# Kernel tuning notes

Measured on AMD Instinct MI355X. Metric: run time of the kernel, lower is better.

## Reference

```python
import jax, jax.numpy as jnp
import numpy as np

B, S, D, H = 4, 2048, 1024, 16
DK = D // H


def setup_inputs() -> dict:
    key = jax.random.key(0)
    ks = jax.random.split(key, 9)
    x = jax.random.normal(ks[0], (B, S, D), dtype=jnp.float32)
    scale = 1.0 / np.sqrt(D)
    wq = jax.random.normal(ks[1], (D, D), dtype=jnp.float32) * scale
    wk = jax.random.normal(ks[2], (D, D), dtype=jnp.float32) * scale
    wv = jax.random.normal(ks[3], (D, D), dtype=jnp.float32) * scale
    wo = jax.random.normal(ks[4], (D, D), dtype=jnp.float32) * scale
    bq = jax.random.normal(ks[5], (D,), dtype=jnp.float32) * 0.01
    bk = jax.random.normal(ks[6], (D,), dtype=jnp.float32) * 0.01
    bv = jax.random.normal(ks[7], (D,), dtype=jnp.float32) * 0.01
    bo = jax.random.normal(ks[8], (D,), dtype=jnp.float32) * 0.01
    # causal mask: True where scores should be masked to -inf (j > i)
    mask = jnp.triu(jnp.ones((S, S), dtype=bool), k=1)[None, None, :, :]
    return {"x": x, "wq": wq, "bq": bq, "wk": wk, "bk": bk,
            "wv": wv, "bv": bv, "wo": wo, "bo": bo, "mask": mask}


def reference(x, wq, bq, wk, bk, wv, bv, wo, bo, mask):
    b, s, _ = x.shape
    # projections
    q = (x @ wq + bq).reshape(b, s, H, DK).transpose(0, 2, 1, 3)  # [B,H,S,DK]
    k = (x @ wk + bk).reshape(b, s, H, DK).transpose(0, 2, 1, 3)
    v = (x @ wv + bv).reshape(b, s, H, DK).transpose(0, 2, 1, 3)
    scores = jnp.einsum("bhqd,bhkd->bhqk", q, k) / np.sqrt(DK)
    scores = jnp.where(mask, -jnp.inf, scores)
    attn = jax.nn.softmax(scores, axis=-1)  # dropout p=0.0 -> identity
    out = jnp.einsum("bhqk,bhkd->bhqd", attn, v)
    out = out.transpose(0, 2, 1, 3).reshape(b, s, D)
    return out @ wo + bo
```

## Files before the change

kernel.cpp:

```cpp
#include <hip/hip_runtime.h>


typedef __attribute__((ext_vector_type(8))) short short8;
typedef __attribute__((ext_vector_type(4))) float floatx4;
typedef __attribute__((ext_vector_type(4))) unsigned short ushort4v;

#define SCLF (0.125f * 1.44269504f)

__device__ __forceinline__ unsigned short f2bf(float f) {
    unsigned int u = __float_as_uint(f);
    unsigned int r = (u + 0x7fffu + ((u >> 16) & 1u)) >> 16;
    return (unsigned short)r;
}

__device__ __forceinline__ unsigned int pk2bf(float lo, float hi) {
    return __builtin_amdgcn_perm(__float_as_uint(hi), __float_as_uint(lo), 0x07060302u);
}

__device__ __forceinline__ void gll16(const unsigned short* g, unsigned short* l) {
    __builtin_amdgcn_global_load_lds(
        (const __attribute__((address_space(1))) unsigned int*)g,
        (__attribute__((address_space(3))) unsigned int*)l, 16, 0, 0);
}

__device__ __forceinline__ void xcd_tile3(int nx, int& m0, int& n0) {
    int lid = blockIdx.y * nx + blockIdx.x;
    int grp = lid & 7;
    int inner = lid >> 3;
    int my = grp * 4 + (inner & 3);
    int mx = inner >> 2;
    m0 = my * 256;
    n0 = mx * 128;
}

__global__ void cvtx_kernel(const float* __restrict__ x, unsigned short* __restrict__ xb) {
    int i = (blockIdx.x * 256 + threadIdx.x) * 4;
    float4 v = *(const float4*)&x[i];
    ushort4v o;
    o.x = f2bf(v.x); o.y = f2bf(v.y); o.z = f2bf(v.z); o.w = f2bf(v.w);
    *(ushort4v*)&xb[i] = o;
}

__global__ void wtrans_kernel(const float* __restrict__ wq, const float* __restrict__ wk,
                              const float* __restrict__ wv, const float* __restrict__ wo,
                              unsigned short* __restrict__ wtbase) {
    __shared__ float t[32][33];
    int z = blockIdx.z;
    const float* w = (z == 0) ? wq : (z == 1) ? wk : (z == 2) ? wv : wo;
    unsigned short* wt = wtbase + ((long)z << 20);
    int kb = blockIdx.y * 32, nb = blockIdx.x * 32;
    int col = threadIdx.x & 31, rw = threadIdx.x >> 5;
#pragma unroll
    for (int i = 0; i < 4; i++) {
        int row = rw + i * 8;
        t[row][col] = w[(kb + row) * 1024 + nb + col];
    }
    __syncthreads();
#pragma unroll
    for (int i = 0; i < 4; i++) {
        int row = rw + i * 8;
        wt[(nb + row) * 1024 + kb + col] = f2bf(t[col][row]);
    }
}

#define ASZ (256 * 64)
#define BSZ (128 * 64)
#define BUFSZ (ASZ + BSZ)

__device__ __forceinline__ short8 ldsr(const unsigned short* p) { return *(const short8*)p; }

template <bool SW>
__device__ __forceinline__ void gemm_core256(const unsigned short* __restrict__ A,
                                             const unsigned short* __restrict__ Bt,
                                             unsigned short* lds,
                                             int m0, int n0, floatx4 (&acc)[8][2]) {
    const int K = 1024, NT = 16;
    int tid = threadIdx.x;
    int lane = tid & 63, wave = tid >> 6;
    int wm = wave >> 2, wn = wave & 3;
    int quad = lane >> 4, l15 = lane & 15, l7 = l15 & 7;
    int rsub = lane >> 3;
    int gl = (lane & 7) ^ rsub;

    floatx4 zero4 = {0.f, 0.f, 0.f, 0.f};
#pragma unroll
    for (int i = 0; i < 8; i++)
#pragma unroll
        for (int j = 0; j < 2; j++) acc[i][j] = zero4;

    auto stage = [&](int kt, int b) {
        const unsigned short* Ag = A + (long)m0 * K + kt * 64;
        const unsigned short* Bg = Bt + (long)n0 * K + kt * 64;
        unsigned short* as = lds + b * BUFSZ;
        unsigned short* bs = as + ASZ;
#pragma unroll
        for (int p = 0; p < 4; p++) {
            int chunk = wave * 4 + p;
            gll16(&Ag[(chunk * 8 + rsub) * K + gl * 8], &as[chunk * 512 + lane * 8]);
        }
#pragma unroll
        for (int p = 0; p < 2; p++) {
            int chunk = wave * 2 + p;
            gll16(&Bg[(chunk * 8 + rsub) * K + gl * 8], &bs[chunk * 512 + lane * 8]);
        }
    };

    stage(0, 0);
    stage(1, 1);
    stage(2, 2);
    asm volatile("s_waitcnt vmcnt(12)" ::: "memory");
    __builtin_amdgcn_s_barrier();
    asm volatile("" ::: "memory");

    int buf = 0;
    for (int kt = 0; kt < NT; kt++) {
        const unsigned short* as = lds + buf * BUFSZ;
        const unsigned short* bs = as + ASZ;
        short8 bf[2][2], af[4][2], ag[4][2];
#pragma unroll
        for (int j = 0; j < 2; j++) {
            int rb = wn * 32 + j * 16 + l15;
#pragma unroll
            for (int kk = 0; kk < 2; kk++)
                bf[j][kk] = ldsr(&bs[rb * 64 + (((kk * 4 + quad) ^ l7) * 8)]);
        }
#pragma unroll
        for (int i = 0; i < 4; i++) {
            int r = wm * 128 + i * 16 + l15;
#pragma unroll
            for (int kk = 0; kk < 2; kk++)
                af[i][kk] = ldsr(&as[r * 64 + (((kk * 4 + quad) ^ l7) * 8)]);
        }
        __builtin_amdgcn_s_setprio(1);
#pragma unroll
        for (int i = 0; i < 4; i++)
#pragma unroll
            for (int j = 0; j < 2; j++)
#pragma unroll
                for (int kk = 0; kk < 2; kk++)
                    acc[i][j] = SW
                        ? __builtin_amdgcn_mfma_f32_16x16x32_bf16(bf[j][kk], af[i][kk], acc[i][j], 0, 0, 0)
                        : __builtin_amdgcn_mfma_f32_16x16x32_bf16(af[i][kk], bf[j][kk], acc[i][j], 0, 0, 0);
        __builtin_amdgcn_s_setprio(0);
#pragma unroll
        for (int i = 0; i < 4; i++) {
            int r = wm * 128 + 64 + i * 16 + l15;
#pragma unroll
            for (int kk = 0; kk < 2; kk++)
                ag[i][kk] = ldsr(&as[r * 64 + (((kk * 4 + quad) ^ l7) * 8)]);
        }
        __builtin_amdgcn_s_setprio(1);
#pragma unroll
        for (int i = 0; i < 4; i++)
#pragma unroll
            for (int j = 0; j < 2; j++)
#pragma unroll
                for (int kk = 0; kk < 2; kk++)
                    acc[4 + i][j] = SW
                        ? __builtin_amdgcn_mfma_f32_16x16x32_bf16(bf[j][kk], ag[i][kk], acc[4 + i][j], 0, 0, 0)
                        : __builtin_amdgcn_mfma_f32_16x16x32_bf16(ag[i][kk], bf[j][kk], acc[4 + i][j], 0, 0, 0);
        __builtin_amdgcn_s_setprio(0);
        asm volatile("" ::: "memory");
        __builtin_amdgcn_s_barrier();
        asm volatile("" ::: "memory");
        if (kt + 3 < NT) {
            stage(kt + 3, buf);
            asm volatile("s_waitcnt vmcnt(12)" ::: "memory");
        } else if (kt + 3 == NT) {
            asm volatile("s_waitcnt vmcnt(6)" ::: "memory");
        } else if (kt + 2 == NT) {
            asm volatile("s_waitcnt vmcnt(0)" ::: "memory");
        }
        __builtin_amdgcn_s_barrier();
        asm volatile("" ::: "memory");
        buf = (buf == 2) ? 0 : buf + 1;
    }
}

__global__ __launch_bounds__(512, 2) void proj_kernel(
    const unsigned short* __restrict__ xb, const unsigned short* __restrict__ wt,
    const float* __restrict__ bq, const float* __restrict__ bk, const float* __restrict__ bv,
    unsigned short* __restrict__ qo, unsigned short* __restrict__ ko,
    unsigned short* __restrict__ vo) {
    extern __shared__ __align__(16) unsigned short smem[];
    int m0, n0;
    xcd_tile3(24, m0, n0);
    int tid = threadIdx.x, lane = tid & 63, wave = tid >> 6;
    int wm = wave >> 2, wn = wave & 3, quad = lane >> 4, l15 = lane & 15;
    floatx4 acc[8][2];

    if (n0 < 2048) {
        gemm_core256<true>(xb, wt, smem, m0, n0, acc);
        int which = n0 >> 10;
        const float* bias = which ? bk : bq;
        unsigned short* dst = which ? ko : qo;
        float sc = which ? 1.0f : SCLF;
#pragma unroll
        for (int mt = 0; mt < 8; mt++)
#pragma unroll
            for (int nt = 0; nt < 2; nt++) {
                int tok = m0 + wm * 128 + mt * 16 + l15;
                int b = tok >> 11, s = tok & 2047;
                int colf = (n0 + wn * 32 + nt * 16 + quad * 4) & 1023;
                float4 bb = *(const float4*)&bias[colf];
                int h = colf >> 6, dk = colf & 63;
                ushort4v o;
                o.x = f2bf((acc[mt][nt][0] + bb.x) * sc);
                o.y = f2bf((acc[mt][nt][1] + bb.y) * sc);
                o.z = f2bf((acc[mt][nt][2] + bb.z) * sc);
                o.w = f2bf((acc[mt][nt][3] + bb.w) * sc);
                *(ushort4v*)&dst[((long)((b * 16 + h) * 2048 + s)) * 64 + dk] = o;
            }
    } else {
        gemm_core256<false>(xb, wt, smem, m0, n0, acc);
#pragma unroll
        for (int mt = 0; mt < 8; mt++)
#pragma unroll
            for (int nt = 0; nt < 2; nt++) {
                int tok0 = m0 + wm * 128 + mt * 16 + quad * 4;
                int b = tok0 >> 11, s = tok0 & 2047;
                int colf = (n0 & 1023) + wn * 32 + nt * 16 + l15;
                int h = colf >> 6, dk = colf & 63;
                float bb = bv[colf];
                ushort4v o;
                o.x = f2bf(acc[mt][nt][0] + bb);
                o.y = f2bf(acc[mt][nt][1] + bb);
                o.z = f2bf(acc[mt][nt][2] + bb);
                o.w = f2bf(acc[mt][nt][3] + bb);
                *(ushort4v*)&vo[((long)((b * 16 + h) * 64 + dk)) * 2048 + s] = o;
            }
    }
}

__global__ __launch_bounds__(512, 2) void gemm_out_kernel(
    const unsigned short* __restrict__ ob, const unsigned short* __restrict__ wto,
    const float* __restrict__ bo, float* __restrict__ out) {
    extern __shared__ __align__(16) unsigned short smem[];
    int m0, n0;
    xcd_tile3(8, m0, n0);
    int tid = threadIdx.x, lane = tid & 63, wave = tid >> 6;
    int wm = wave >> 2, wn = wave & 3, quad = lane >> 4, l15 = lane & 15;
    floatx4 acc[8][2];
    gemm_core256<true>(ob, wto, smem, m0, n0, acc);

#pragma unroll
    for (int mt = 0; mt < 8; mt++)
#pragma unroll
        for (int nt = 0; nt < 2; nt++) {
            int tok = m0 + wm * 128 + mt * 16 + l15;
            int cg = n0 + wn * 32 + nt * 16 + quad * 4;
            float4 bb = *(const float4*)&bo[cg];
            float4 o;
            o.x = acc[mt][nt][0] + bb.x;
            o.y = acc[mt][nt][1] + bb.y;
            o.z = acc[mt][nt][2] + bb.z;
            o.w = acc[mt][nt][3] + bb.w;
            *(float4*)&out[(long)tok * 1024 + cg] = o;
        }
}

__device__ __forceinline__ void stage_kv(const unsigned short* __restrict__ Kg,
                                         const unsigned short* __restrict__ Vg,
                                         unsigned short* Ks, unsigned short* Vs,
                                         int lane, int wave) {
    int rsub = lane >> 3;
    int g = (lane & 7) ^ rsub;
#pragma unroll
    for (int p = 0; p < 2; p++) {
        int chunk = wave * 2 + p;
        int r = chunk * 8 + rsub;
        gll16(&Kg[r * 64 + g * 8], &Ks[chunk * 512]);
        gll16(&Vg[r * 2048 + g * 8], &Vs[chunk * 512]);
    }
}

__global__ __launch_bounds__(256, 4) void attn_kernel(
    const unsigned short* __restrict__ Q, const unsigned short* __restrict__ Kk,
    const unsigned short* __restrict__ Vt, unsigned short* __restrict__ O) {
    __shared__ __align__(16) unsigned short Ks[2][8 * 512];
    __shared__ __align__(16) unsigned short Vs[2][8 * 512];
    __shared__ __align__(16) unsigned short Ps[4 * 16 * 64];

    int bid = blockIdx.x;
    int qt = 15 - (bid >> 6);
    int bh = bid & 63;
    int q0 = qt * 128;
    long base = (long)bh * 2048 * 64;
    long vbase = (long)bh * 64 * 2048;
    int tid = threadIdx.x, lane = tid & 63, wave = tid >> 6;
    int quad = lane >> 4, l15 = lane & 15, l7 = l15 & 7;

    short8 qfA[2], qfB[2];
    int qrA = q0 + wave * 16 + l15;
    int qrB = qrA + 64;
    qfA[0] = *(const short8*)&Q[base + qrA * 64 + quad * 8];
    qfA[1] = *(const short8*)&Q[base + qrA * 64 + 32 + quad * 8];
    qfB[0] = *(const short8*)&Q[base + qrB * 64 + quad * 8];
    qfB[1] = *(const short8*)&Q[base + qrB * 64 + 32 + quad * 8];

    float lA = 0.f, lB = 0.f;
    floatx4 oA[4], oB[4];
    floatx4 zero4 = {0.f, 0.f, 0.f, 0.f};
#pragma unroll
    for (int st = 0; st < 4; st++) { oA[st] = zero4; oB[st] = zero4; }

    unsigned short* myP = &Ps[(wave * 16) * 64];
    int pw_off = l15 * 64 + (quad & 1) * 4;
    int pr0 = l15 * 64 + ((quad ^ l7) * 8);
    int pr1 = l15 * 64 + (((4 + quad) ^ l7) * 8);

    int ktmax = 2 * qt + 1;
    stage_kv(&Kk[base], &Vt[vbase], Ks[0], Vs[0], lane, wave);
    __syncthreads();

    for (int kt = 0; kt <= ktmax; kt++) {
        int cur = kt & 1;
        if (kt < ktmax)
            stage_kv(&Kk[base + (long)(kt + 1) * 64 * 64], &Vt[vbase + (kt + 1) * 64],
                     Ks[cur ^ 1], Vs[cur ^ 1], lane, wave);
        bool doA = (kt < ktmax);
        bool maskA = (kt == ktmax - 1);
        bool maskB = (kt == ktmax);

        floatx4 saA[4], saB[4];
#pragma unroll
        for (int st = 0; st < 4; st++) {
            int row = st * 16 + l15;
            short8 kf0 = ldsr(&Ks[cur][row * 64 + ((quad ^ l7) * 8)]);
            short8 kf1 = ldsr(&Ks[cur][row * 64 + (((4 + quad) ^ l7) * 8)]);
            saB[st] = __builtin_amdgcn_mfma_f32_16x16x32_bf16(kf0, qfB[0], zero4, 0, 0, 0);
            saB[st] = __builtin_amdgcn_mfma_f32_16x16x32_bf16(kf1, qfB[1], saB[st], 0, 0, 0);
            if (doA) {
                saA[st] = __builtin_amdgcn_mfma_f32_16x16x32_bf16(kf0, qfA[0], zero4, 0, 0, 0);
                saA[st] = __builtin_amdgcn_mfma_f32_16x16x32_bf16(kf1, qfA[1], saA[st], 0, 0, 0);
            }
        }

        int kg0 = kt * 64 + quad * 4;
        short8 pfB0, pfB1, pfA0, pfA1;
        {
            float p[4][4];
#pragma unroll
            for (int st = 0; st < 4; st++)
#pragma unroll
                for (int r = 0; r < 4; r++)
                    p[st][r] = __builtin_amdgcn_exp2f(saB[st][r]);
            if (maskB) {
#pragma unroll
                for (int st = 0; st < 4; st++)
#pragma unroll
                    for (int r = 0; r < 4; r++)
                        if (kg0 + st * 16 + r > qrB) p[st][r] = 0.f;
            }
            float rs = 0.f;
#pragma unroll
            for (int st = 0; st < 4; st++) {
                rs += p[st][0] + p[st][1] + p[st][2] + p[st][3];
                uint2 pw;
                pw.x = pk2bf(p[st][0], p[st][1]);
                pw.y = pk2bf(p[st][2], p[st][3]);
                *(uint2*)&myP[pw_off + (((st * 2 + (quad >> 1)) ^ l7) * 8)] = pw;
            }
            rs += __shfl_xor(rs, 16, 64);
            rs += __shfl_xor(rs, 32, 64);
            lB += rs;
            pfB0 = ldsr(&myP[pr0]);
            pfB1 = ldsr(&myP[pr1]);
        }
        if (doA) {
            float p[4][4];
#pragma unroll
            for (int st = 0; st < 4; st++)
#pragma unroll
                for (int r = 0; r < 4; r++)
                    p[st][r] = __builtin_amdgcn_exp2f(saA[st][r]);
            if (maskA) {
#pragma unroll
                for (int st = 0; st < 4; st++)
#pragma unroll
                    for (int r = 0; r < 4; r++)
                        if (kg0 + st * 16 + r > qrA) p[st][r] = 0.f;
            }
            float rs = 0.f;
#pragma unroll
            for (int st = 0; st < 4; st++) {
                rs += p[st][0] + p[st][1] + p[st][2] + p[st][3];
                uint2 pw;
                pw.x = pk2bf(p[st][0], p[st][1]);
                pw.y = pk2bf(p[st][2], p[st][3]);
                *(uint2*)&myP[pw_off + (((st * 2 + (quad >> 1)) ^ l7) * 8)] = pw;
            }
            rs += __shfl_xor(rs, 16, 64);
            rs += __shfl_xor(rs, 32, 64);
            lA += rs;
            pfA0 = ldsr(&myP[pr0]);
            pfA1 = ldsr(&myP[pr1]);
        }

#pragma unroll
        for (int st = 0; st < 4; st++) {
            int row = st * 16 + l15;
            short8 vf0 = ldsr(&Vs[cur][row * 64 + ((quad ^ l7) * 8)]);
            short8 vf1 = ldsr(&Vs[cur][row * 64 + (((4 + quad) ^ l7) * 8)]);
            oB[st] = __builtin_amdgcn_mfma_f32_16x16x32_bf16(vf0, pfB0, oB[st], 0, 0, 0);
            oB[st] = __builtin_amdgcn_mfma_f32_16x16x32_bf16(vf1, pfB1, oB[st], 0, 0, 0);
            if (doA) {
                oA[st] = __builtin_amdgcn_mfma_f32_16x16x32_bf16(vf0, pfA0, oA[st], 0, 0, 0);
                oA[st] = __builtin_amdgcn_mfma_f32_16x16x32_bf16(vf1, pfA1, oA[st], 0, 0, 0);
            }
        }
        __syncthreads();
    }

    int b = bh >> 4, h = bh & 15;
    float invA = 1.f / lA, invB = 1.f / lB;
#pragma unroll
    for (int st = 0; st < 4; st++) {
        uint2 ov;
        ov.x = pk2bf(oA[st][0] * invA, oA[st][1] * invA);
        ov.y = pk2bf(oA[st][2] * invA, oA[st][3] * invA);
        *(uint2*)&O[((long)(b * 2048 + qrA)) * 1024 + h * 64 + st * 16 + quad * 4] = ov;
        uint2 ow;
        ow.x = pk2bf(oB[st][0] * invB, oB[st][1] * invB);
        ow.y = pk2bf(oB[st][2] * invB, oB[st][3] * invB);
        *(uint2*)&O[((long)(b * 2048 + qrB)) * 1024 + h * 64 + st * 16 + quad * 4] = ow;
    }
}

extern "C" void kernel_launch(void* const* d_in, const int* in_sizes, int n_in,
                              void* d_out, int out_size, void* d_ws, size_t ws_size,
                              hipStream_t stream) {
    const float* x  = (const float*)d_in[0];
    const float* wq = (const float*)d_in[1];
    const float* bq = (const float*)d_in[2];
    const float* wk = (const float*)d_in[3];
    const float* bk = (const float*)d_in[4];
    const float* wv = (const float*)d_in[5];
    const float* bv = (const float*)d_in[6];
    const float* wo = (const float*)d_in[7];
    const float* bo = (const float*)d_in[8];

    char* w = (char*)d_ws;
    unsigned short* xb  = (unsigned short*)w;
    unsigned short* wtq = (unsigned short*)(w + (16u << 20));
    unsigned short* wto = wtq + (3u << 20);
    unsigned short* qb  = wto + (1u << 20);
    unsigned short* kb  = qb + (8u << 20);
    unsigned short* vb  = kb + (8u << 20);
    unsigned short* ob  = vb + (8u << 20);

    cvtx_kernel<<<8192, 256, 0, stream>>>(x, xb);
    wtrans_kernel<<<dim3(32, 32, 4), 256, 0, stream>>>(wq, wk, wv, wo, wtq);
    proj_kernel<<<dim3(24, 32), 512, 144 * 1024, stream>>>(xb, wtq, bq, bk, bv, qb, kb, vb);
    attn_kernel<<<1024, 256, 0, stream>>>(qb, kb, vb, ob);
    gemm_out_kernel<<<dim3(8, 32), 512, 144 * 1024, stream>>>(ob, wto, bo, (float*)d_out);
}
```

Before: 265.8 us.

## Reshape GEMM warp tiling to 4x2 waves with 64x64 per-wave tiles

The GEMM core changes the wave layout from 2x4 (128x32 per wave) to 4x2 (64x64 per wave). Each wave now needs fewer LDS fragment loads per MFMA (8 fragments for 16 MFMAs per k-half instead of 12 for 16). The k-loop is split into two phases, each with an added block barrier and an explicit lgkmcnt wait before the MFMAs. This lowers LDS read traffic but adds barriers per k-tile, which may cost synchronization overhead.

Result: no change. 265.5 us (-0.1%).

```diff
diff --git a/kernel.cpp b/kernel.cpp
--- a/kernel.cpp
+++ b/kernel.cpp
@@ -73,20 +73,20 @@
 __device__ __forceinline__ void gemm_core256(const unsigned short* __restrict__ A,
                                              const unsigned short* __restrict__ Bt,
                                              unsigned short* lds,
-                                             int m0, int n0, floatx4 (&acc)[8][2]) {
+                                             int m0, int n0, floatx4 (&acc)[4][4]) {
     const int K = 1024, NT = 16;
     int tid = threadIdx.x;
     int lane = tid & 63, wave = tid >> 6;
-    int wm = wave >> 2, wn = wave & 3;
+    int wm = wave >> 1, wn = wave & 1;
     int quad = lane >> 4, l15 = lane & 15, l7 = l15 & 7;
     int rsub = lane >> 3;
     int gl = (lane & 7) ^ rsub;
 
     floatx4 zero4 = {0.f, 0.f, 0.f, 0.f};
 #pragma unroll
-    for (int i = 0; i < 8; i++)
-#pragma unroll
-        for (int j = 0; j < 2; j++) acc[i][j] = zero4;
+    for (int i = 0; i < 4; i++)
+#pragma unroll
+        for (int j = 0; j < 4; j++) acc[i][j] = zero4;
 
     auto stage = [&](int kt, int b) {
         const unsigned short* Ag = A + (long)m0 * K + kt * 64;
@@ -116,53 +116,36 @@
     for (int kt = 0; kt < NT; kt++) {
         const unsigned short* as = lds + buf * BUFSZ;
         const unsigned short* bs = as + ASZ;
-        short8 bf[2][2], af[4][2], ag[4][2];
-#pragma unroll
-        for (int j = 0; j < 2; j++) {
-            int rb = wn * 32 + j * 16 + l15;
-#pragma unroll
-            for (int kk = 0; kk < 2; kk++)
-                bf[j][kk] = ldsr(&bs[rb * 64 + (((kk * 4 + quad) ^ l7) * 8)]);
-        }
-#pragma unroll
-        for (int i = 0; i < 4; i++) {
-            int r = wm * 128 + i * 16 + l15;
-#pragma unroll
-            for (int kk = 0; kk < 2; kk++)
-                af[i][kk] = ldsr(&as[r * 64 + (((kk * 4 + quad) ^ l7) * 8)]);
-        }
-        __builtin_amdgcn_s_setprio(1);
-#pragma unroll
-        for (int i = 0; i < 4; i++)
-#pragma unroll
-            for (int j = 0; j < 2; j++)
-#pragma unroll
-                for (int kk = 0; kk < 2; kk++)
+#pragma unroll
+        for (int ph = 0; ph < 2; ph++) {
+            short8 af[4], bf[4];
+#pragma unroll
+            for (int i = 0; i < 4; i++) {
+                int r = wm * 64 + i * 16 + l15;
+                af[i] = ldsr(&as[r * 64 + (((ph * 4 + quad) ^ l7) * 8)]);
+            }
+#pragma unroll
+            for (int j = 0; j < 4; j++) {
+                int rb = wn * 64 + j * 16 + l15;
+                bf[j] = ldsr(&bs[rb * 64 + (((ph * 4 + quad) ^ l7) * 8)]);
+            }
+            asm volatile("" ::: "memory");
+            __builtin_amdgcn_s_barrier();
+            asm volatile("s_waitcnt lgkmcnt(0)" ::: "memory");
+            __builtin_amdgcn_sched_barrier(0);
+            __builtin_amdgcn_s_setprio(1);
+#pragma unroll
+            for (int i = 0; i < 4; i++)
+#pragma unroll
+                for (int j = 0; j < 4; j++)
                     acc[i][j] = SW
-                        ? __builtin_amdgcn_mfma_f32_16x16x32_bf16(bf[j][kk], af[i][kk], acc[i][j], 0, 0, 0)
-                        : __builtin_amdgcn_mfma_f32_16x16x32_bf16(af[i][kk], bf[j][kk], acc[i][j], 0, 0, 0);
-        __builtin_amdgcn_s_setprio(0);
-#pragma unroll
-        for (int i = 0; i < 4; i++) {
-            int r = wm * 128 + 64 + i * 16 + l15;
-#pragma unroll
-            for (int kk = 0; kk < 2; kk++)
-                ag[i][kk] = ldsr(&as[r * 64 + (((kk * 4 + quad) ^ l7) * 8)]);
-        }
-        __builtin_amdgcn_s_setprio(1);
-#pragma unroll
-        for (int i = 0; i < 4; i++)
-#pragma unroll
-            for (int j = 0; j < 2; j++)
-#pragma unroll
-                for (int kk = 0; kk < 2; kk++)
-                    acc[4 + i][j] = SW
-                        ? __builtin_amdgcn_mfma_f32_16x16x32_bf16(bf[j][kk], ag[i][kk], acc[4 + i][j], 0, 0, 0)
-                        : __builtin_amdgcn_mfma_f32_16x16x32_bf16(ag[i][kk], bf[j][kk], acc[4 + i][j], 0, 0, 0);
-        __builtin_amdgcn_s_setprio(0);
-        asm volatile("" ::: "memory");
-        __builtin_amdgcn_s_barrier();
-        asm volatile("" ::: "memory");
+                        ? __builtin_amdgcn_mfma_f32_16x16x32_bf16(bf[j], af[i], acc[i][j], 0, 0, 0)
+                        : __builtin_amdgcn_mfma_f32_16x16x32_bf16(af[i], bf[j], acc[i][j], 0, 0, 0);
+            __builtin_amdgcn_s_setprio(0);
+            asm volatile("" ::: "memory");
+            __builtin_amdgcn_s_barrier();
+            asm volatile("" ::: "memory");
+        }
         if (kt + 3 < NT) {
             stage(kt + 3, buf);
             asm volatile("s_waitcnt vmcnt(12)" ::: "memory");
@@ -186,8 +169,8 @@
     int m0, n0;
     xcd_tile3(24, m0, n0);
     int tid = threadIdx.x, lane = tid & 63, wave = tid >> 6;
-    int wm = wave >> 2, wn = wave & 3, quad = lane >> 4, l15 = lane & 15;
-    floatx4 acc[8][2];
+    int wm = wave >> 1, wn = wave & 1, quad = lane >> 4, l15 = lane & 15;
+    floatx4 acc[4][4];
 
     if (n0 < 2048) {
         gemm_core256<true>(xb, wt, smem, m0, n0, acc);
@@ -196,12 +179,12 @@
         unsigned short* dst = which ? ko : qo;
         float sc = which ? 1.0f : SCLF;
 #pragma unroll
-        for (int mt = 0; mt < 8; mt++)
-#pragma unroll
-            for (int nt = 0; nt < 2; nt++) {
-                int tok = m0 + wm * 128 + mt * 16 + l15;
+        for (int mt = 0; mt < 4; mt++)
+#pragma unroll
+            for (int nt = 0; nt < 4; nt++) {
+                int tok = m0 + wm * 64 + mt * 16 + l15;
                 int b = tok >> 11, s = tok & 2047;
-                int colf = (n0 + wn * 32 + nt * 16 + quad * 4) & 1023;
+                int colf = (n0 + wn * 64 + nt * 16 + quad * 4) & 1023;
                 float4 bb = *(const float4*)&bias[colf];
                 int h = colf >> 6, dk = colf & 63;
                 ushort4v o;
@@ -214,12 +197,12 @@
     } else {
         gemm_core256<false>(xb, wt, smem, m0, n0, acc);
 #pragma unroll
-        for (int mt = 0; mt < 8; mt++)
-#pragma unroll
-            for (int nt = 0; nt < 2; nt++) {
-                int tok0 = m0 + wm * 128 + mt * 16 + quad * 4;
+        for (int mt = 0; mt < 4; mt++)
+#pragma unroll
+            for (int nt = 0; nt < 4; nt++) {
+                int tok0 = m0 + wm * 64 + mt * 16 + quad * 4;
                 int b = tok0 >> 11, s = tok0 & 2047;
-                int colf = (n0 & 1023) + wn * 32 + nt * 16 + l15;
+                int colf = (n0 & 1023) + wn * 64 + nt * 16 + l15;
                 int h = colf >> 6, dk = colf & 63;
                 float bb = bv[colf];
                 ushort4v o;
@@ -239,16 +222,16 @@
     int m0, n0;
     xcd_tile3(8, m0, n0);
     int tid = threadIdx.x, lane = tid & 63, wave = tid >> 6;
-    int wm = wave >> 2, wn = wave & 3, quad = lane >> 4, l15 = lane & 15;
-    floatx4 acc[8][2];
+    int wm = wave >> 1, wn = wave & 1, quad = lane >> 4, l15 = lane & 15;
+    floatx4 acc[4][4];
     gemm_core256<true>(ob, wto, smem, m0, n0, acc);
 
 #pragma unroll
-    for (int mt = 0; mt < 8; mt++)
-#pragma unroll
-        for (int nt = 0; nt < 2; nt++) {
-            int tok = m0 + wm * 128 + mt * 16 + l15;
-            int cg = n0 + wn * 32 + nt * 16 + quad * 4;
+    for (int mt = 0; mt < 4; mt++)
+#pragma unroll
+        for (int nt = 0; nt < 4; nt++) {
+            int tok = m0 + wm * 64 + mt * 16 + l15;
+            int cg = n0 + wn * 64 + nt * 16 + quad * 4;
             float4 bb = *(const float4*)&bo[cg];
             float4 o;
             o.x = acc[mt][nt][0] + bb.x;
```

## Switch projection and output GEMMs to 256x256 tiles with double-buffered half-staging

Applied to the files above, without the earlier changes.

Moves the projection and output GEMMs from 256x128 tiles to square 256x256 tiles, so each wave computes a 128x64 sub-tile with more MFMAs per loaded fragment. The three-stage ring buffer becomes a two-buffer scheme in which A and B halves are staged piecewise between four MFMA phases, synchronised with extra barriers and lgkmcnt waits. This aims to raise arithmetic intensity and cut global and LDS traffic per flop. In exchange the block count halves (384 and 128 blocks) and register pressure grows from 64 to 128 accumulator floats, which may reduce occupancy and load balance, especially for the output GEMM's 128 blocks.

Measured after the change: 275.3 us. 3.6% more time.

```diff
diff --git a/kernel.cpp b/kernel.cpp
--- a/kernel.cpp
+++ b/kernel.cpp
@@ -23,14 +23,14 @@
         (__attribute__((address_space(3))) unsigned int*)l, 16, 0, 0);
 }
 
-__device__ __forceinline__ void xcd_tile3(int nx, int& m0, int& n0) {
+__device__ __forceinline__ void xcd_tile4(int nx, int& m0, int& n0) {
     int lid = blockIdx.y * nx + blockIdx.x;
     int grp = lid & 7;
     int inner = lid >> 3;
-    int my = grp * 4 + (inner & 3);
-    int mx = inner >> 2;
+    int my = grp * 4 + inner / nx;
+    int mx = inner % nx;
     m0 = my * 256;
-    n0 = mx * 128;
+    n0 = mx * 256;
 }
 
 __global__ void cvtx_kernel(const float* __restrict__ x, unsigned short* __restrict__ xb) {
@@ -64,16 +64,15 @@
 }
 
 #define ASZ (256 * 64)
-#define BSZ (128 * 64)
-#define BUFSZ (ASZ + BSZ)
+#define BUFSZ (2 * ASZ)
 
 __device__ __forceinline__ short8 ldsr(const unsigned short* p) { return *(const short8*)p; }
 
 template <bool SW>
-__device__ __forceinline__ void gemm_core256(const unsigned short* __restrict__ A,
-                                             const unsigned short* __restrict__ Bt,
-                                             unsigned short* lds,
-                                             int m0, int n0, floatx4 (&acc)[8][2]) {
+__device__ __forceinline__ void gemm_core256sq(const unsigned short* __restrict__ A,
+                                               const unsigned short* __restrict__ Bt,
+                                               unsigned short* lds,
+                                               int m0, int n0, floatx4 (&acc)[8][4]) {
     const int K = 1024, NT = 16;
     int tid = threadIdx.x;
     int lane = tid & 63, wave = tid >> 6;
@@ -86,51 +85,56 @@
 #pragma unroll
     for (int i = 0; i < 8; i++)
 #pragma unroll
-        for (int j = 0; j < 2; j++) acc[i][j] = zero4;
-
-    auto stage = [&](int kt, int b) {
+        for (int j = 0; j < 4; j++) acc[i][j] = zero4;
+
+    auto stageA = [&](int kt, int half) {
         const unsigned short* Ag = A + (long)m0 * K + kt * 64;
+        unsigned short* as = lds + (kt & 1) * BUFSZ;
+#pragma unroll
+        for (int p = 0; p < 2; p++) {
+            int chunk = half * 16 + wave * 2 + p;
+            gll16(&Ag[(chunk * 8 + rsub) * K + gl * 8], &as[chunk * 512 + lane * 8]);
+        }
+    };
+    auto stageB = [&](int kt, int half) {
         const unsigned short* Bg = Bt + (long)n0 * K + kt * 64;
-        unsigned short* as = lds + b * BUFSZ;
-        unsigned short* bs = as + ASZ;
-#pragma unroll
-        for (int p = 0; p < 4; p++) {
-            int chunk = wave * 4 + p;
-            gll16(&Ag[(chunk * 8 + rsub) * K + gl * 8], &as[chunk * 512 + lane * 8]);
-        }
+        unsigned short* bs = lds + (kt & 1) * BUFSZ + ASZ;
 #pragma unroll
         for (int p = 0; p < 2; p++) {
-            int chunk = wave * 2 + p;
+            int chunk = half * 16 + wave * 2 + p;
             gll16(&Bg[(chunk * 8 + rsub) * K + gl * 8], &bs[chunk * 512 + lane * 8]);
         }
     };
 
-    stage(0, 0);
-    stage(1, 1);
-    stage(2, 2);
-    asm volatile("s_waitcnt vmcnt(12)" ::: "memory");
+    stageA(0, 0); stageA(0, 1); stageB(0, 0); stageB(0, 1);
+    stageB(1, 0); stageA(1, 0); stageB(1, 1);
+    asm volatile("s_waitcnt vmcnt(6)" ::: "memory");
     __builtin_amdgcn_s_barrier();
     asm volatile("" ::: "memory");
 
-    int buf = 0;
+    short8 af[4][2], b0[2][2], b1[2][2];
+
     for (int kt = 0; kt < NT; kt++) {
-        const unsigned short* as = lds + buf * BUFSZ;
+        const unsigned short* as = lds + (kt & 1) * BUFSZ;
         const unsigned short* bs = as + ASZ;
-        short8 bf[2][2], af[4][2], ag[4][2];
-#pragma unroll
-        for (int j = 0; j < 2; j++) {
-            int rb = wn * 32 + j * 16 + l15;
-#pragma unroll
-            for (int kk = 0; kk < 2; kk++)
-                bf[j][kk] = ldsr(&bs[rb * 64 + (((kk * 4 + quad) ^ l7) * 8)]);
-        }
+
 #pragma unroll
         for (int i = 0; i < 4; i++) {
             int r = wm * 128 + i * 16 + l15;
-#pragma unroll
-            for (int kk = 0; kk < 2; kk++)
-                af[i][kk] = ldsr(&as[r * 64 + (((kk * 4 + quad) ^ l7) * 8)]);
-        }
+            af[i][0] = ldsr(&as[r * 64 + ((quad ^ l7) * 8)]);
+            af[i][1] = ldsr(&as[r * 64 + (((4 + quad) ^ l7) * 8)]);
+        }
+#pragma unroll
+        for (int j = 0; j < 2; j++) {
+            int r = wn * 64 + j * 16 + l15;
+            b0[j][0] = ldsr(&bs[r * 64 + ((quad ^ l7) * 8)]);
+            b0[j][1] = ldsr(&bs[r * 64 + (((4 + quad) ^ l7) * 8)]);
+        }
+        if (kt + 1 < NT) stageA(kt + 1, 1);
+        asm volatile("" ::: "memory");
+        __builtin_amdgcn_s_barrier();
+        asm volatile("s_waitcnt lgkmcnt(0)" ::: "memory");
+        __builtin_amdgcn_sched_barrier(0);
         __builtin_amdgcn_s_setprio(1);
 #pragma unroll
         for (int i = 0; i < 4; i++)
@@ -139,16 +143,65 @@
 #pragma unroll
                 for (int kk = 0; kk < 2; kk++)
                     acc[i][j] = SW
-                        ? __builtin_amdgcn_mfma_f32_16x16x32_bf16(bf[j][kk], af[i][kk], acc[i][j], 0, 0, 0)
-                        : __builtin_amdgcn_mfma_f32_16x16x32_bf16(af[i][kk], bf[j][kk], acc[i][j], 0, 0, 0);
+                        ? __builtin_amdgcn_mfma_f32_16x16x32_bf16(b0[j][kk], af[i][kk], acc[i][j], 0, 0, 0)
+                        : __builtin_amdgcn_mfma_f32_16x16x32_bf16(af[i][kk], b0[j][kk], acc[i][j], 0, 0, 0);
         __builtin_amdgcn_s_setprio(0);
+        asm volatile("" ::: "memory");
+        __builtin_amdgcn_s_barrier();
+        asm volatile("" ::: "memory");
+
+#pragma unroll
+        for (int j = 0; j < 2; j++) {
+            int r = wn * 64 + (2 + j) * 16 + l15;
+            b1[j][0] = ldsr(&bs[r * 64 + ((quad ^ l7) * 8)]);
+            b1[j][1] = ldsr(&bs[r * 64 + (((4 + quad) ^ l7) * 8)]);
+        }
+        asm volatile("" ::: "memory");
+        __builtin_amdgcn_s_barrier();
+        asm volatile("s_waitcnt lgkmcnt(0)" ::: "memory");
+        __builtin_amdgcn_sched_barrier(0);
+        __builtin_amdgcn_s_setprio(1);
+#pragma unroll
+        for (int i = 0; i < 4; i++)
+#pragma unroll
+            for (int j = 0; j < 2; j++)
+#pragma unroll
+                for (int kk = 0; kk < 2; kk++)
+                    acc[i][2 + j] = SW
+                        ? __builtin_amdgcn_mfma_f32_16x16x32_bf16(b1[j][kk], af[i][kk], acc[i][2 + j], 0, 0, 0)
+                        : __builtin_amdgcn_mfma_f32_16x16x32_bf16(af[i][kk], b1[j][kk], acc[i][2 + j], 0, 0, 0);
+        __builtin_amdgcn_s_setprio(0);
+        asm volatile("" ::: "memory");
+        __builtin_amdgcn_s_barrier();
+        asm volatile("" ::: "memory");
+
 #pragma unroll
         for (int i = 0; i < 4; i++) {
             int r = wm * 128 + 64 + i * 16 + l15;
-#pragma unroll
-            for (int kk = 0; kk < 2; kk++)
-                ag[i][kk] = ldsr(&as[r * 64 + (((kk * 4 + quad) ^ l7) * 8)]);
-        }
+            af[i][0] = ldsr(&as[r * 64 + ((quad ^ l7) * 8)]);
+            af[i][1] = ldsr(&as[r * 64 + (((4 + quad) ^ l7) * 8)]);
+        }
+        if (kt + 2 < NT) stageB(kt + 2, 0);
+        asm volatile("" ::: "memory");
+        __builtin_amdgcn_s_barrier();
+        asm volatile("s_waitcnt lgkmcnt(0)" ::: "memory");
+        __builtin_amdgcn_sched_barrier(0);
+        __builtin_amdgcn_s_setprio(1);
+#pragma unroll
+        for (int i = 0; i < 4; i++)
+#pragma unroll
+            for (int j = 0; j < 2; j++)
+#pragma unroll
+                for (int kk = 0; kk < 2; kk++)
+                    acc[4 + i][2 + j] = SW
+                        ? __builtin_amdgcn_mfma_f32_16x16x32_bf16(b1[j][kk], af[i][kk], acc[4 + i][2 + j], 0, 0, 0)
+                        : __builtin_amdgcn_mfma_f32_16x16x32_bf16(af[i][kk], b1[j][kk], acc[4 + i][2 + j], 0, 0, 0);
+        __builtin_amdgcn_s_setprio(0);
+        asm volatile("" ::: "memory");
+        __builtin_amdgcn_s_barrier();
+        asm volatile("" ::: "memory");
+
+        if (kt + 2 < NT) { stageA(kt + 2, 0); stageB(kt + 2, 1); }
         __builtin_amdgcn_s_setprio(1);
 #pragma unroll
         for (int i = 0; i < 4; i++)
@@ -157,23 +210,16 @@
 #pragma unroll
                 for (int kk = 0; kk < 2; kk++)
                     acc[4 + i][j] = SW
-                        ? __builtin_amdgcn_mfma_f32_16x16x32_bf16(bf[j][kk], ag[i][kk], acc[4 + i][j], 0, 0, 0)
-                        : __builtin_amdgcn_mfma_f32_16x16x32_bf16(ag[i][kk], bf[j][kk], acc[4 + i][j], 0, 0, 0);
+                        ? __builtin_amdgcn_mfma_f32_16x16x32_bf16(b0[j][kk], af[i][kk], acc[4 + i][j], 0, 0, 0)
+                        : __builtin_amdgcn_mfma_f32_16x16x32_bf16(af[i][kk], b0[j][kk], acc[4 + i][j], 0, 0, 0);
         __builtin_amdgcn_s_setprio(0);
-        asm volatile("" ::: "memory");
-        __builtin_amdgcn_s_barrier();
-        asm volatile("" ::: "memory");
-        if (kt + 3 < NT) {
-            stage(kt + 3, buf);
-            asm volatile("s_waitcnt vmcnt(12)" ::: "memory");
-        } else if (kt + 3 == NT) {
+        if (kt + 2 < NT) {
             asm volatile("s_waitcnt vmcnt(6)" ::: "memory");
-        } else if (kt + 2 == NT) {
+        } else if (kt + 1 < NT) {
             asm volatile("s_waitcnt vmcnt(0)" ::: "memory");
         }
         __builtin_amdgcn_s_barrier();
         asm volatile("" ::: "memory");
-        buf = (buf == 2) ? 0 : buf + 1;
     }
 }
 
@@ -184,13 +230,13 @@
     unsigned short* __restrict__ vo) {
     extern __shared__ __align__(16) unsigned short smem[];
     int m0, n0;
-    xcd_tile3(24, m0, n0);
+    xcd_tile4(12, m0, n0);
     int tid = threadIdx.x, lane = tid & 63, wave = tid >> 6;
     int wm = wave >> 2, wn = wave & 3, quad = lane >> 4, l15 = lane & 15;
-    floatx4 acc[8][2];
+    floatx4 acc[8][4];
 
     if (n0 < 2048) {
-        gemm_core256<true>(xb, wt, smem, m0, n0, acc);
+        gemm_core256sq<true>(xb, wt, smem, m0, n0, acc);
         int which = n0 >> 10;
         const float* bias = which ? bk : bq;
         unsigned short* dst = which ? ko : qo;
@@ -198,10 +244,10 @@
 #pragma unroll
         for (int mt = 0; mt < 8; mt++)
 #pragma unroll
-            for (int nt = 0; nt < 2; nt++) {
+            for (int nt = 0; nt < 4; nt++) {
                 int tok = m0 + wm * 128 + mt * 16 + l15;
                 int b = tok >> 11, s = tok & 2047;
-                int colf = (n0 + wn * 32 + nt * 16 + quad * 4) & 1023;
+                int colf = (n0 + wn * 64 + nt * 16 + quad * 4) & 1023;
                 float4 bb = *(const float4*)&bias[colf];
                 int h = colf >> 6, dk = colf & 63;
                 ushort4v o;
@@ -212,14 +258,14 @@
                 *(ushort4v*)&dst[((long)((b * 16 + h) * 2048 + s)) * 64 + dk] = o;
             }
     } else {
-        gemm_core256<false>(xb, wt, smem, m0, n0, acc);
+        gemm_core256sq<false>(xb, wt, smem, m0, n0, acc);
 #pragma unroll
         for (int mt = 0; mt < 8; mt++)
 #pragma unroll
-            for (int nt = 0; nt < 2; nt++) {
+            for (int nt = 0; nt < 4; nt++) {
                 int tok0 = m0 + wm * 128 + mt * 16 + quad * 4;
                 int b = tok0 >> 11, s = tok0 & 2047;
-                int colf = (n0 & 1023) + wn * 32 + nt * 16 + l15;
+                int colf = (n0 & 1023) + wn * 64 + nt * 16 + l15;
                 int h = colf >> 6, dk = colf & 63;
                 float bb = bv[colf];
                 ushort4v o;
@@ -237,18 +283,18 @@
     const float* __restrict__ bo, float* __restrict__ out) {
     extern __shared__ __align__(16) unsigned short smem[];
     int m0, n0;
-    xcd_tile3(8, m0, n0);
+    xcd_tile4(4, m0, n0);
     int tid = threadIdx.x, lane = tid & 63, wave = tid >> 6;
     int wm = wave >> 2, wn = wave & 3, quad = lane >> 4, l15 = lane & 15;
-    floatx4 acc[8][2];
-    gemm_core256<true>(ob, wto, smem, m0, n0, acc);
+    floatx4 acc[8][4];
+    gemm_core256sq<true>(ob, wto, smem, m0, n0, acc);
 
 #pragma unroll
     for (int mt = 0; mt < 8; mt++)
 #pragma unroll
-        for (int nt = 0; nt < 2; nt++) {
+        for (int nt = 0; nt < 4; nt++) {
             int tok = m0 + wm * 128 + mt * 16 + l15;
-            int cg = n0 + wn * 32 + nt * 16 + quad * 4;
+            int cg = n0 + wn * 64 + nt * 16 + quad * 4;
             float4 bb = *(const float4*)&bo[cg];
             float4 o;
             o.x = acc[mt][nt][0] + bb.x;
@@ -451,7 +497,7 @@
 
     cvtx_kernel<<<8192, 256, 0, stream>>>(x, xb);
     wtrans_kernel<<<dim3(32, 32, 4), 256, 0, stream>>>(wq, wk, wv, wo, wtq);
-    proj_kernel<<<dim3(24, 32), 512, 144 * 1024, stream>>>(xb, wtq, bq, bk, bv, qb, kb, vb);
+    proj_kernel<<<dim3(12, 32), 512, 128 * 1024, stream>>>(xb, wtq, bq, bk, bv, qb, kb, vb);
     attn_kernel<<<1024, 256, 0, stream>>>(qb, kb, vb, ob);
-    gemm_out_kernel<<<dim3(8, 32), 512, 144 * 1024, stream>>>(ob, wto, bo, (float*)d_out);
-}
+    gemm_out_kernel<<<dim3(4, 32), 512, 128 * 1024, stream>>>(ob, wto, bo, (float*)d_out);
+}
```
